# Optimization experiments

Measured on AMD Instinct MI355X. Metric: run time of the kernel, lower is better.

## Reference

```python
import jax, jax.numpy as jnp
import numpy as np

DIM = 320; HEADS = 8; DHEAD = 40; CTX_DIM = 768
INNER = HEADS * DHEAD; FF_INNER = 4 * DIM
B = 1; N = 4096; M = 77
SCALE = DHEAD ** -0.5


def setup_inputs() -> dict:
    key = jax.random.key(0)
    ks = jax.random.split(key, 16)
    p = lambda i, shape: jax.random.normal(ks[i], shape, dtype=jnp.float32) * 0.02
    return {
        "x": jax.random.normal(ks[0], (B, N, DIM), dtype=jnp.float32),
        "context": jax.random.normal(ks[1], (B, M, CTX_DIM), dtype=jnp.float32),
        "focused_attention_mask": jax.random.uniform(ks[2], (1, M, M), dtype=jnp.float32),
        "g1": jnp.ones((DIM,), jnp.float32), "b1": jnp.zeros((DIM,), jnp.float32),
        "g2": jnp.ones((DIM,), jnp.float32), "b2": jnp.zeros((DIM,), jnp.float32),
        "g3": jnp.ones((DIM,), jnp.float32), "b3": jnp.zeros((DIM,), jnp.float32),
        "Wq1": p(3, (DIM, INNER)), "Wk1": p(4, (DIM, INNER)), "Wv1": p(5, (DIM, INNER)),
        "Wo1": p(6, (INNER, DIM)), "bo1": jnp.zeros((DIM,), jnp.float32),
        "Wq2": p(7, (DIM, INNER)), "Wk2": p(8, (CTX_DIM, INNER)), "Wv2": p(9, (CTX_DIM, INNER)),
        "Wo2": p(10, (INNER, DIM)), "bo2": jnp.zeros((DIM,), jnp.float32),
        "Wff1": p(11, (DIM, 2 * FF_INNER)), "bff1": jnp.zeros((2 * FF_INNER,), jnp.float32),
        "Wff2": p(12, (FF_INNER, DIM)), "bff2": jnp.zeros((DIM,), jnp.float32),
        "use_fca": 1,
    }


def _ln(x, g, b):
    mu = x.mean(-1, keepdims=True)
    var = jnp.mean((x - mu) ** 2, -1, keepdims=True)
    return (x - mu) * jax.lax.rsqrt(var + 1e-5) * g + b


def _attn(xn, ctx, Wq, Wk, Wv, Wo, bo, fam, use_fca):
    b, n, _ = xn.shape
    heads = lambda t: t.reshape(b, t.shape[1], HEADS, DHEAD).transpose(0, 2, 1, 3)  # b h n d
    q, k, v = heads(xn @ Wq), heads(ctx @ Wk), heads(ctx @ Wv)
    sim = jnp.einsum('bhid,bhjd->bhij', q, k) * SCALE
    if use_fca:
        m = fam.shape[-1]  # fam: [1, m, m], batch must be 1 (repeat_interleave semantics)
        fw = jnp.einsum('bhqk,dk->bhqd', sim[..., :m], fam[0])
        fw = jnp.minimum(jnp.abs(fw), 1.0)
        fw = fw / (jnp.max(fw, axis=-1, keepdims=True) + 1e-6)
        fw = (fw > 0.6).astype(sim.dtype)
        sim = sim.at[..., :m].add((fw - 1.0) * 50.0)
    a = jax.nn.softmax(sim, axis=-1)
    o = jnp.einsum('bhij,bhjd->bhid', a, v).transpose(0, 2, 1, 3).reshape(b, n, INNER)
    return o @ Wo + bo


def reference(x, context, focused_attention_mask,
              g1, b1, g2, b2, g3, b3,
              Wq1, Wk1, Wv1, Wo1, bo1,
              Wq2, Wk2, Wv2, Wo2, bo2,
              Wff1, bff1, Wff2, bff2, use_fca):
    # attn1: self-attention (context=None in original -> use_fca forced to 0)
    h1 = _ln(x, g1, b1)
    x = _attn(h1, h1, Wq1, Wk1, Wv1, Wo1, bo1, None, 0) + x
    # attn2: cross-attention with focused-attention mask
    h2 = _ln(x, g2, b2)
    x = _attn(h2, context, Wq2, Wk2, Wv2, Wo2, bo2, focused_attention_mask, int(use_fca)) + x
    # GEGLU feed-forward
    h3 = _ln(x, g3, b3)
    proj = h3 @ Wff1 + bff1
    a_, gate = jnp.split(proj, 2, axis=-1)
    x = (a_ * jax.nn.gelu(gate, approximate=False)) @ Wff2 + bff2 + x
    return x
```

## Files before the change

### kernel.cpp

```cpp
#include <hip/hip_runtime.h>
#include <math.h>

typedef __bf16 bf16_t;
typedef __bf16 bf16x8 __attribute__((ext_vector_type(8)));
typedef __bf16 bf16x4 __attribute__((ext_vector_type(4)));
typedef float  f32x4  __attribute__((ext_vector_type(4)));
typedef _Float16 f16_t;
typedef _Float16 f16x4 __attribute__((ext_vector_type(4)));
typedef _Float16 f16x8 __attribute__((ext_vector_type(8)));
typedef __fp16 hf16x2 __attribute__((ext_vector_type(2)));

static constexpr float ATT_SCALE = 0.15811388300841897f;
static constexpr float SC2 = 0.22811031f;
static constexpr float LOG2E = 1.4426950408889634f;

__device__ __forceinline__ bf16_t f2b(float f) {
  unsigned u = __float_as_uint(f);
  u = (u + 0x7fffu + ((u >> 16) & 1u)) >> 16;
  unsigned short s = (unsigned short)u;
  bf16_t r;
  *(unsigned short*)&r = s;
  return r;
}
__device__ __forceinline__ float b2f(bf16_t b) {
  unsigned short s = *(const unsigned short*)&b;
  return __uint_as_float(((unsigned)s) << 16);
}
__device__ __forceinline__ void sto(float v, float* p)  { *p = v; }
__device__ __forceinline__ void sto(float v, bf16_t* p) { *p = f2b(v); }
__device__ __forceinline__ unsigned pkh2(float a, float b) {
  hf16x2 h = __builtin_amdgcn_cvt_pkrtz(a, b);
  return *(unsigned*)&h;
}

__global__ __launch_bounds__(256) void prep_kernel(
    const float* __restrict__ Wq1, const float* __restrict__ Wk1, const float* __restrict__ Wv1,
    const float* __restrict__ Wo1, const float* __restrict__ Wq2,
    const float* __restrict__ Wk2, const float* __restrict__ Wv2, const float* __restrict__ Wo2,
    const float* __restrict__ Wff1, const float* __restrict__ Wff2,
    const float* __restrict__ fam,
    bf16_t* __restrict__ wqkvt, bf16_t* __restrict__ wo1t, float* __restrict__ wkv2t,
    bf16_t* __restrict__ wo2t, bf16_t* __restrict__ wff1t, bf16_t* __restrict__ wff2t,
    bf16_t* __restrict__ wq2th, bf16_t* __restrict__ wq2tl,
    bf16_t* __restrict__ famh, bf16_t* __restrict__ faml,
    bf16_t* __restrict__ zpad)
{
  const int T1 = 960*320;
  const int T2 = T1 + 320*320;
  const int T3 = T2 + 768*640;
  const int T4 = T3 + 320*320;
  const int T5 = T4 + 2560*320;
  const int T6 = T5 + 320*1280;
  const int T7 = T6 + 320*320;
  const int T8 = T7 + 96*96;
  const int T9 = T8 + 135168;
  for (int i = blockIdx.x*256 + threadIdx.x; i < T9; i += gridDim.x*256) {
    if (i < T1) {
      int n = i / 320, k = i - n*320;
      float v = (n < 320) ? Wq1[k*320+n] * SC2
              : (n < 640) ? Wk1[k*320+n-320] : Wv1[k*320+n-640];
      wqkvt[i] = f2b(v);
    } else if (i < T2) {
      int e = i - T1; int n = e / 320, k = e - n*320;
      wo1t[e] = f2b(Wo1[k*320+n]);
    } else if (i < T3) {
      int e = i - T2; int n = e / 768, k = e - n*768;
      wkv2t[e] = (n < 320) ? Wk2[k*320+n] : Wv2[k*320+n-320];
    } else if (i < T4) {
      int e = i - T3; int n = e / 320, k = e - n*320;
      wo2t[e] = f2b(Wo2[k*320+n]);
    } else if (i < T5) {
      int e = i - T4; int n = e / 320, k = e - n*320;
      wff1t[e] = f2b(Wff1[(size_t)k*2560+n]);
    } else if (i < T6) {
      int e = i - T5; int n = e / 1280, k = e - n*1280;
      wff2t[e] = f2b(Wff2[k*320+n]);
    } else if (i < T7) {
      int e = i - T6; int n = e / 320, k = e - n*320;
      float v = Wq2[k*320+n];
      bf16_t h = f2b(v);
      wq2th[e] = h;
      wq2tl[e] = f2b(v - b2f(h));
    } else if (i < T8) {
      int e = i - T7; int d = e / 96, k = e - d*96;
      float v = (d < 77 && k < 77) ? fam[d*77 + k] : 0.f;
      bf16_t h = f2b(v);
      famh[e] = h;
      faml[e] = f2b(v - b2f(h));
    } else {
      zpad[i - T8] = f2b(0.f);
    }
  }
}

template<typename OT>
__global__ __launch_bounds__(256) void ln_kernel(
    const float* __restrict__ x, const float* __restrict__ g, const float* __restrict__ b,
    OT* __restrict__ out)
{
  const int lane = threadIdx.x & 63;
  const int row = blockIdx.x * 4 + (threadIdx.x >> 6);
  const float* xr = x + (size_t)row * 320;
  float v[5], s = 0.f, s2 = 0.f;
#pragma unroll
  for (int i = 0; i < 5; i++) { v[i] = xr[lane + i*64]; s += v[i]; s2 += v[i]*v[i]; }
#pragma unroll
  for (int o = 32; o; o >>= 1) { s += __shfl_xor(s, o); s2 += __shfl_xor(s2, o); }
  float mu = s * (1.f/320.f);
  float rs = rsqrtf(fmaxf(s2*(1.f/320.f) - mu*mu, 0.f) + 1e-5f);
#pragma unroll
  for (int i = 0; i < 5; i++) {
    int c = lane + i*64;
    sto((v[i]-mu)*rs*g[c] + b[c], &out[(size_t)row*320 + c]);
  }
}

__global__ __launch_bounds__(256) void ln2_split_kernel(
    const float* __restrict__ x, const float* __restrict__ g, const float* __restrict__ b,
    bf16_t* __restrict__ hi, bf16_t* __restrict__ lo)
{
  const int lane = threadIdx.x & 63;
  const int row = blockIdx.x * 4 + (threadIdx.x >> 6);
  const float* xr = x + (size_t)row * 320;
  float v[5], s = 0.f, s2 = 0.f;
#pragma unroll
  for (int i = 0; i < 5; i++) { v[i] = xr[lane + i*64]; s += v[i]; s2 += v[i]*v[i]; }
#pragma unroll
  for (int o = 32; o; o >>= 1) { s += __shfl_xor(s, o); s2 += __shfl_xor(s2, o); }
  float mu = s * (1.f/320.f);
  float rs = rsqrtf(fmaxf(s2*(1.f/320.f) - mu*mu, 0.f) + 1e-5f);
#pragma unroll
  for (int i = 0; i < 5; i++) {
    int c = lane + i*64;
    float y = (v[i]-mu)*rs*g[c] + b[c];
    bf16_t h = f2b(y);
    hi[(size_t)row*320 + c] = h;
    lo[(size_t)row*320 + c] = f2b(y - b2f(h));
  }
}

__global__ __launch_bounds__(256) void kv2_dot_kernel(
    const float* __restrict__ ctx, const float* __restrict__ wkv2t,
    bf16_t* __restrict__ k2h, bf16_t* __restrict__ k2l, bf16_t* __restrict__ v2t)
{
  const int gid = blockIdx.x*16 + (threadIdx.x >> 4);
  const int q = threadIdx.x & 15;
  const int m = gid / 640, n = gid - m*640;
  const float4* a = (const float4*)(ctx + (size_t)m*768);
  const float4* b = (const float4*)(wkv2t + (size_t)n*768);
  float acc = 0.f;
#pragma unroll
  for (int i = 0; i < 12; i++) {
    float4 av = a[i*16+q], bv = b[i*16+q];
    acc += av.x*bv.x + av.y*bv.y + av.z*bv.z + av.w*bv.w;
  }
#pragma unroll
  for (int o = 8; o; o >>= 1) acc += __shfl_xor(acc, o);
  if (q == 0) {
    if (n < 320) {
      int h = n / 40, d = n - h*40;
      int i = h*6144 + m*64 + d;
      bf16_t hh = f2b(acc);
      k2h[i] = hh;
      k2l[i] = f2b(acc - b2f(hh));
    } else {
      int n2 = n - 320; int h = n2 / 40, d = n2 - h*40;
      v2t[h*4608 + d*96 + m] = f2b(acc);
    }
  }
}

__global__ __launch_bounds__(256) void repack_vt_kernel(
    const bf16_t* __restrict__ qkvb, f16_t* __restrict__ vpack, bf16_t* __restrict__ kpack)
{
  __shared__ f16_t T[64*44];
  const int tid = threadIdx.x;
  const int t0 = blockIdx.x * 64, h = blockIdx.y;
  for (int e = tid; e < 320; e += 256) {
    int t = e / 5, c8 = (e - t*5) * 8;
    bf16x8 v = *(const bf16x8*)(qkvb + (size_t)(t0+t)*960 + 640 + h*40 + c8);
    f16_t* dst = &T[t*44 + c8];
#pragma unroll
    for (int j = 0; j < 8; j++) dst[j] = (f16_t)b2f(v[j]);
  }
  __syncthreads();
  for (int e = tid; e < 3072; e += 256) {
    int dt = e >> 10;
    int r  = e & 1023;
    int g2 = r >> 9, o = r & 511;
    int lane = o >> 3, j = o & 7;
    int qd = lane >> 4, ln = lane & 15;
    int d = dt*16 + ln;
    int key = g2*32 + ((j & 4) ? 16 : 0) + qd*4 + (j & 3);
    float val;
    if (d < 40)       val = (float)T[key*44 + d];
    else if (d == 40) val = 1.0f;
    else              val = 0.0f;
    vpack[(((size_t)h*3 + dt)*128 + (t0 >> 5) + g2)*512 + o] = (f16_t)val;
  }
  for (int e = tid; e < 2560; e += 256) {
    int g = e / 640, o = e - g*640;
    int key = t0 + g*16;
    bf16_t val;
    if (o < 512) {
      int lane = o >> 3, j = o & 7;
      int qd = lane >> 4, ln = lane & 15;
      val = qkvb[(size_t)(key + ln)*960 + 320 + h*40 + qd*8 + j];
    } else {
      int o2 = o - 512; int ln = o2 >> 3, j = o2 & 7;
      val = qkvb[(size_t)(key + ln)*960 + 320 + h*40 + 32 + j];
    }
    kpack[((size_t)h*256 + (t0 >> 4) + g)*640 + o] = val;
  }
}

__global__ __launch_bounds__(512, 4) void flash_self_kernel(
    const bf16_t* __restrict__ qkvb, const bf16_t* __restrict__ kpack,
    const f16_t* __restrict__ vpack,
    bf16_t* __restrict__ o1a)
{
  __shared__ float Red[12288];
  const int tid = threadIdx.x;
  const int w = tid >> 6, lane = tid & 63;
  const int ln = lane & 15, qd = lane >> 4;
  const int qh = w >> 2, kh = w & 3;
  const int h = blockIdx.x & 7;
  const int q0 = (blockIdx.x >> 3) * 64;

  const int kgbase = h*256 + kh*2;
  const int vgbase = h*384 + kh;
  const int lko = lane*8;

  bf16x8 zero8 = {};
  bf16x8 bq[2][2];
#pragma unroll
  for (int nt = 0; nt < 2; nt++) {
    const bf16_t* qp = qkvb + (size_t)(q0 + qh*32 + nt*16 + ln)*960 + h*40;
    bq[nt][0] = *(const bf16x8*)(qp + qd*8);
    bq[nt][1] = (qd == 0) ? *(const bf16x8*)(qp + 32) : zero8;
  }

  f32x4 zero4 = {0.f,0.f,0.f,0.f};
  f32x4 oacc[3][2];
#pragma unroll
  for (int a = 0; a < 3; a++)
#pragma unroll
    for (int b = 0; b < 2; b++) oacc[a][b] = zero4;

#define FS_LOADK(DST, K0)                                                       \
  {                                                                             \
    const bf16_t* kp_ = kpack + ((size_t)kgbase + ((K0) >> 4)) * 640;           \
    DST[0][0] = *(const bf16x8*)(kp_ + lko);                                    \
    DST[0][1] = (qd == 0) ? *(const bf16x8*)(kp_ + 512 + ln*8) : zero8;         \
    DST[1][0] = *(const bf16x8*)(kp_ + 640 + lko);                              \
    DST[1][1] = (qd == 0) ? *(const bf16x8*)(kp_ + 1152 + ln*8) : zero8;        \
  }

#define FS_LOADV(DST, K0)                                                       \
  {                                                                             \
    _Pragma("unroll")                                                           \
    for (int dt_ = 0; dt_ < 3; dt_++)                                           \
      DST[dt_] = *(const f16x8*)(vpack + ((size_t)vgbase + dt_*128 + ((K0) >> 5)) * 512 + lko); \
  }

#define FS_COMPUTE(KA, VA)                                                      \
  {                                                                             \
    _Pragma("unroll")                                                           \
    for (int nt = 0; nt < 2; nt++) {                                            \
      f32x4 s0 = __builtin_amdgcn_mfma_f32_16x16x32_bf16(KA[0][0], bq[nt][0], zero4, 0,0,0); \
      s0 = __builtin_amdgcn_mfma_f32_16x16x32_bf16(KA[0][1], bq[nt][1], s0, 0,0,0); \
      f32x4 s1 = __builtin_amdgcn_mfma_f32_16x16x32_bf16(KA[1][0], bq[nt][0], zero4, 0,0,0); \
      s1 = __builtin_amdgcn_mfma_f32_16x16x32_bf16(KA[1][1], bq[nt][1], s1, 0,0,0); \
      uint4 u_;                                                                 \
      u_.x = pkh2(__builtin_amdgcn_exp2f(s0[0]), __builtin_amdgcn_exp2f(s0[1])); \
      u_.y = pkh2(__builtin_amdgcn_exp2f(s0[2]), __builtin_amdgcn_exp2f(s0[3])); \
      u_.z = pkh2(__builtin_amdgcn_exp2f(s1[0]), __builtin_amdgcn_exp2f(s1[1])); \
      u_.w = pkh2(__builtin_amdgcn_exp2f(s1[2]), __builtin_amdgcn_exp2f(s1[3])); \
      f16x8 pb = *(f16x8*)&u_;                                                  \
      _Pragma("unroll")                                                         \
      for (int dt = 0; dt < 3; dt++)                                            \
        oacc[dt][nt] = __builtin_amdgcn_mfma_f32_16x16x32_f16(VA[dt], pb, oacc[dt][nt], 0,0,0); \
    }                                                                           \
  }

  bf16x8 ka[2][2], kb[2][2];
  f16x8 va[3], vb[3];
  FS_LOADK(ka, 0);
  FS_LOADV(va, 0);
#pragma unroll 1
  for (int it = 0; it < 32; it += 2) {
    const int k0 = it*128;
    FS_LOADK(kb, k0 + 128);
    FS_LOADV(vb, k0 + 128);
    FS_COMPUTE(ka, va);
    FS_LOADK(ka, (it + 2 < 32) ? (k0 + 256) : 0);
    FS_LOADV(va, (it + 2 < 32) ? (k0 + 256) : 0);
    FS_COMPUTE(kb, vb);
  }
#undef FS_LOADK
#undef FS_LOADV
#undef FS_COMPUTE

#pragma unroll
  for (int nt = 0; nt < 2; nt++)
#pragma unroll
    for (int dt = 0; dt < 3; dt++)
      *(f32x4*)&Red[((w*2 + nt)*3 + dt)*256 + ln*16 + qd*4] = oacc[dt][nt];
  __syncthreads();
  const int dgrp = tid & 7, lq = (tid >> 3) & 15, ntw = (tid >> 7) & 1, qh2 = tid >> 8;
  float l = Red[(((qh2*4 + 0)*2 + ntw)*3 + 2)*256 + lq*16 + 8]
          + Red[(((qh2*4 + 1)*2 + ntw)*3 + 2)*256 + lq*16 + 8]
          + Red[(((qh2*4 + 2)*2 + ntw)*3 + 2)*256 + lq*16 + 8]
          + Red[(((qh2*4 + 3)*2 + ntw)*3 + 2)*256 + lq*16 + 8];
  float inv = 1.f / l;
  bf16_t* obase = o1a + (size_t)(q0 + qh2*32 + ntw*16 + lq)*320 + h*40;
#pragma unroll
  for (int i = 0; i < 5; i++) {
    int d = dgrp + i*8;
    int dt = d >> 4, dr = d & 15;
    float o = Red[(((qh2*4 + 0)*2 + ntw)*3 + dt)*256 + lq*16 + dr]
            + Red[(((qh2*4 + 1)*2 + ntw)*3 + dt)*256 + lq*16 + dr]
            + Red[(((qh2*4 + 2)*2 + ntw)*3 + dt)*256 + lq*16 + dr]
            + Red[(((qh2*4 + 3)*2 + ntw)*3 + dt)*256 + lq*16 + dr];
    obase[d] = f2b(o * inv);
  }
}

__global__ __launch_bounds__(256) void attn_cross_kernel(
    const float* __restrict__ q2, const bf16_t* __restrict__ k2h, const bf16_t* __restrict__ k2l,
    const bf16_t* __restrict__ famh, const bf16_t* __restrict__ faml,
    const bf16_t* __restrict__ v2t, const int* __restrict__ use_fca,
    bf16_t* __restrict__ o2)
{
  __shared__ bf16_t SMh[4][16*96];
  __shared__ bf16_t SMl[4][16*96];
  __shared__ bf16_t PAs[4][16*96];
  const int tid = threadIdx.x;
  const int w = tid >> 6, lane = tid & 63;
  const int ln = lane & 15, qd = lane >> 4;
  const int h = blockIdx.x & 7;
  const int q0 = (blockIdx.x >> 3)*64 + w*16;
  const int fca = use_fca[0];
  bf16_t* smh = SMh[w];
  bf16_t* sml = SMl[w];
  bf16_t* pa  = PAs[w];

  {
    bf16x4 z = {};
    int q = lane >> 2, c = 80 + (lane & 3)*4;
    *(bf16x4*)&smh[q*96 + c] = z;
    *(bf16x4*)&sml[q*96 + c] = z;
    *(bf16x4*)&pa [q*96 + c] = z;
  }

  bf16x8 zero8 = {};
  bf16x8 aqh0, aql0, aqh1 = zero8, aql1 = zero8;
  {
    const float* qp = q2 + (size_t)(q0 + ln)*320 + h*40;
    float4 v0 = *(const float4*)(qp + qd*8);
    float4 v1 = *(const float4*)(qp + qd*8 + 4);
    float qv[8] = {v0.x,v0.y,v0.z,v0.w,v1.x,v1.y,v1.z,v1.w};
#pragma unroll
    for (int i = 0; i < 8; i++) {
      bf16_t hh = f2b(qv[i]);
      aqh0[i] = hh; aql0[i] = f2b(qv[i] - b2f(hh));
    }
    if (qd == 0) {
      float4 u0 = *(const float4*)(qp + 32);
      float4 u1 = *(const float4*)(qp + 36);
      float uv[8] = {u0.x,u0.y,u0.z,u0.w,u1.x,u1.y,u1.z,u1.w};
#pragma unroll
      for (int i = 0; i < 8; i++) {
        bf16_t hh = f2b(uv[i]);
        aqh1[i] = hh; aql1[i] = f2b(uv[i] - b2f(hh));
      }
    }
  }

  f32x4 zero4 = {0.f,0.f,0.f,0.f};
  float ss[5][4];
#pragma unroll
  for (int nt = 0; nt < 5; nt++) {
    const bf16_t* kb = k2h + ((size_t)h*96 + nt*16 + ln)*64 + qd*8;
    const bf16_t* kl = k2l + ((size_t)h*96 + nt*16 + ln)*64 + qd*8;
    bf16x8 kh0 = *(const bf16x8*)kb;
    bf16x8 kh1 = *(const bf16x8*)(kb + 32);
    bf16x8 kl0 = *(const bf16x8*)kl;
    bf16x8 kl1 = *(const bf16x8*)(kl + 32);
    f32x4 s;
    s = __builtin_amdgcn_mfma_f32_16x16x32_bf16(aqh0, kl0, zero4, 0, 0, 0);
    s = __builtin_amdgcn_mfma_f32_16x16x32_bf16(aql0, kh0, s, 0, 0, 0);
    s = __builtin_amdgcn_mfma_f32_16x16x32_bf16(aqh0, kh0, s, 0, 0, 0);
    s = __builtin_amdgcn_mfma_f32_16x16x32_bf16(aqh1, kl1, s, 0, 0, 0);
    s = __builtin_amdgcn_mfma_f32_16x16x32_bf16(aql1, kh1, s, 0, 0, 0);
    s = __builtin_amdgcn_mfma_f32_16x16x32_bf16(aqh1, kh1, s, 0, 0, 0);
#pragma unroll
    for (int r = 0; r < 4; r++) {
      float sv = s[r] * ATT_SCALE;
      ss[nt][r] = sv;
      bf16_t hh = f2b(sv);
      smh[(qd*4 + r)*96 + nt*16 + ln] = hh;
      sml[(qd*4 + r)*96 + nt*16 + ln] = f2b(sv - b2f(hh));
    }
  }

  f32x4 facc[5];
#pragma unroll
  for (int nt = 0; nt < 5; nt++) facc[nt] = zero4;
#pragma unroll
  for (int c = 0; c < 3; c++) {
    bf16x8 sah = *(const bf16x8*)&smh[ln*96 + c*32 + qd*8];
    bf16x8 sal = *(const bf16x8*)&sml[ln*96 + c*32 + qd*8];
#pragma unroll
    for (int nt = 0; nt < 5; nt++) {
      bf16x8 fh8 = *(const bf16x8*)(famh + ((size_t)(nt*16 + ln))*96 + c*32 + qd*8);
      bf16x8 fl8 = *(const bf16x8*)(faml + ((size_t)(nt*16 + ln))*96 + c*32 + qd*8);
      facc[nt] = __builtin_amdgcn_mfma_f32_16x16x32_bf16(sah, fl8, facc[nt], 0, 0, 0);
      facc[nt] = __builtin_amdgcn_mfma_f32_16x16x32_bf16(sal, fh8, facc[nt], 0, 0, 0);
      facc[nt] = __builtin_amdgcn_mfma_f32_16x16x32_bf16(sah, fh8, facc[nt], 0, 0, 0);
    }
  }

  float pr[5][4];
  if (fca) {
    float fwv[5][4], fm[4];
#pragma unroll
    for (int nt = 0; nt < 5; nt++)
#pragma unroll
      for (int r = 0; r < 4; r++) fwv[nt][r] = fminf(fabsf(facc[nt][r]), 1.f);
#pragma unroll
    for (int r = 0; r < 4; r++) {
      float m = fmaxf(fmaxf(fwv[0][r], fwv[1][r]), fmaxf(fwv[2][r], fmaxf(fwv[3][r], fwv[4][r])));
#pragma unroll
      for (int o = 8; o; o >>= 1) m = fmaxf(m, __shfl_xor(m, o));
      fm[r] = m;
    }
#pragma unroll
    for (int nt = 0; nt < 5; nt++)
#pragma unroll
      for (int r = 0; r < 4; r++) {
        float lg = ss[nt][r] - ((fwv[nt][r] > 0.6f*(fm[r] + 1e-6f)) ? 0.f : 50.f);
        pr[nt][r] = __builtin_amdgcn_exp2f(lg * LOG2E);
      }
  } else {
#pragma unroll
    for (int nt = 0; nt < 5; nt++)
#pragma unroll
      for (int r = 0; r < 4; r++)
        pr[nt][r] = __builtin_amdgcn_exp2f(ss[nt][r] * LOG2E);
  }
  if (ln >= 13) {
#pragma unroll
    for (int r = 0; r < 4; r++) pr[4][r] = 0.f;
  }
  float l_[4] = {0.f,0.f,0.f,0.f};
#pragma unroll
  for (int nt = 0; nt < 5; nt++)
#pragma unroll
    for (int r = 0; r < 4; r++) {
      l_[r] += pr[nt][r];
      pa[(qd*4 + r)*96 + nt*16 + ln] = f2b(pr[nt][r]);
    }
#pragma unroll
  for (int r = 0; r < 4; r++)
#pragma unroll
    for (int o = 8; o; o >>= 1) l_[r] += __shfl_xor(l_[r], o);

  f32x4 oacc[3];
#pragma unroll
  for (int nt = 0; nt < 3; nt++) oacc[nt] = zero4;
#pragma unroll
  for (int c = 0; c < 3; c++) {
    bf16x8 paf = *(const bf16x8*)&pa[ln*96 + c*32 + qd*8];
#pragma unroll
    for (int nt = 0; nt < 3; nt++) {
      bf16x8 vb = *(const bf16x8*)(v2t + ((size_t)h*48 + nt*16 + ln)*96 + c*32 + qd*8);
      oacc[nt] = __builtin_amdgcn_mfma_f32_16x16x32_bf16(paf, vb, oacc[nt], 0, 0, 0);
    }
  }
  float inv[4];
#pragma unroll
  for (int r = 0; r < 4; r++) inv[r] = 1.f / l_[r];
#pragma unroll
  for (int nt = 0; nt < 3; nt++) {
    int d = nt*16 + ln;
    if (d < 40) {
#pragma unroll
      for (int r = 0; r < 4; r++)
        o2[(size_t)(q0 + qd*4 + r)*320 + h*40 + d] = f2b(oacc[nt][r]*inv[r]);
    }
  }
}

template<int OUT_BF16>
__global__ __launch_bounds__(256) void gemm_bf16_kernel(
    const bf16_t* __restrict__ A, const bf16_t* __restrict__ Bt,
    const float* __restrict__ bias, const float* __restrict__ resid,
    void* __restrict__ Cout, int M, int N, int K)
{
  __shared__ bf16_t As[128][72];
  __shared__ bf16_t Bs[64][72];
  const int tid = threadIdx.x;
  const int m0 = blockIdx.x * 128, n0 = blockIdx.y * 64;
  const int w = tid >> 6, lane = tid & 63;
  const int wr = w >> 1, wc = w & 1;
  const int ln = lane & 15, qd = lane >> 4;
  f32x4 zero = {0.f, 0.f, 0.f, 0.f};
  f32x4 acc[4][2];
#pragma unroll
  for (int a = 0; a < 4; a++)
#pragma unroll
    for (int b = 0; b < 2; b++) acc[a][b] = zero;

  for (int k0 = 0; k0 < K; k0 += 64) {
    __syncthreads();
#pragma unroll
    for (int i = 0; i < 4; i++) {
      int vid = tid + i*256;
      int r = vid >> 3, c8 = (vid & 7) * 8;
      *(bf16x8*)&As[r][c8] = *(const bf16x8*)(A + (size_t)(m0+r)*K + k0 + c8);
    }
#pragma unroll
    for (int i = 0; i < 2; i++) {
      int vid = tid + i*256;
      int r = vid >> 3, c8 = (vid & 7) * 8;
      *(bf16x8*)&Bs[r][c8] = *(const bf16x8*)(Bt + (size_t)(n0+r)*K + k0 + c8);
    }
    __syncthreads();
#pragma unroll
    for (int c = 0; c < 2; c++) {
      bf16x8 af[4], bfr[2];
#pragma unroll
      for (int mt = 0; mt < 4; mt++)
        af[mt] = *(const bf16x8*)&As[wr*64 + mt*16 + ln][c*32 + qd*8];
#pragma unroll
      for (int nt = 0; nt < 2; nt++)
        bfr[nt] = *(const bf16x8*)&Bs[wc*32 + nt*16 + ln][c*32 + qd*8];
#pragma unroll
      for (int mt = 0; mt < 4; mt++)
#pragma unroll
        for (int nt = 0; nt < 2; nt++)
          acc[mt][nt] = __builtin_amdgcn_mfma_f32_16x16x32_bf16(af[mt], bfr[nt], acc[mt][nt], 0, 0, 0);
    }
  }
#pragma unroll
  for (int mt = 0; mt < 4; mt++)
#pragma unroll
    for (int nt = 0; nt < 2; nt++)
#pragma unroll
      for (int r = 0; r < 4; r++) {
        int gm = m0 + wr*64 + mt*16 + qd*4 + r;
        int gn = n0 + wc*32 + nt*16 + ln;
        float v = acc[mt][nt][r];
        if (bias)  v += bias[gn];
        if (resid) v += resid[(size_t)gm*N + gn];
        if (OUT_BF16) sto(v, &((bf16_t*)Cout)[(size_t)gm*N + gn]);
        else          sto(v, &((float*)Cout)[(size_t)gm*N + gn]);
      }
}

template<int OUT_BF16>
__global__ __launch_bounds__(256) void gemm_bf16_32_kernel(
    const bf16_t* __restrict__ A, const bf16_t* __restrict__ Bt,
    const float* __restrict__ bias, const float* __restrict__ resid,
    void* __restrict__ Cout, int M, int N, int K)
{
  __shared__ bf16_t As[32][72];
  __shared__ bf16_t Bs[64][72];
  const int tid = threadIdx.x;
  const int m0 = blockIdx.x * 32, n0 = blockIdx.y * 64;
  const int w = tid >> 6, lane = tid & 63;
  const int wr = w >> 1, wc = w & 1;
  const int ln = lane & 15, qd = lane >> 4;
  f32x4 zero = {0.f, 0.f, 0.f, 0.f};
  f32x4 acc[2];
  acc[0] = zero; acc[1] = zero;

  for (int k0 = 0; k0 < K; k0 += 64) {
    __syncthreads();
    {
      int r = tid >> 3, c8 = (tid & 7) * 8;
      *(bf16x8*)&As[r][c8] = *(const bf16x8*)(A + (size_t)(m0+r)*K + k0 + c8);
    }
#pragma unroll
    for (int i = 0; i < 2; i++) {
      int vid = tid + i*256;
      int r = vid >> 3, c8 = (vid & 7) * 8;
      *(bf16x8*)&Bs[r][c8] = *(const bf16x8*)(Bt + (size_t)(n0+r)*K + k0 + c8);
    }
    __syncthreads();
#pragma unroll
    for (int c = 0; c < 2; c++) {
      bf16x8 af = *(const bf16x8*)&As[wr*16 + ln][c*32 + qd*8];
#pragma unroll
      for (int nt = 0; nt < 2; nt++) {
        bf16x8 bfr = *(const bf16x8*)&Bs[wc*32 + nt*16 + ln][c*32 + qd*8];
        acc[nt] = __builtin_amdgcn_mfma_f32_16x16x32_bf16(af, bfr, acc[nt], 0, 0, 0);
      }
    }
  }
#pragma unroll
  for (int nt = 0; nt < 2; nt++)
#pragma unroll
    for (int r = 0; r < 4; r++) {
      int gm = m0 + wr*16 + qd*4 + r;
      int gn = n0 + wc*32 + nt*16 + ln;
      float v = acc[nt][r];
      if (bias)  v += bias[gn];
      if (resid) v += resid[(size_t)gm*N + gn];
      if (OUT_BF16) sto(v, &((bf16_t*)Cout)[(size_t)gm*N + gn]);
      else          sto(v, &((float*)Cout)[(size_t)gm*N + gn]);
    }
}

__global__ __launch_bounds__(256) void gemm3_32_kernel(
    const bf16_t* __restrict__ Ah, const bf16_t* __restrict__ Al,
    const bf16_t* __restrict__ Bth, const bf16_t* __restrict__ Btl,
    float* __restrict__ C, int M, int N, int K)
{
  __shared__ bf16_t Ash[32][72];
  __shared__ bf16_t Asl[32][72];
  __shared__ bf16_t Bsh[64][72];
  __shared__ bf16_t Bsl[64][72];
  const int tid = threadIdx.x;
  const int m0 = blockIdx.x * 32, n0 = blockIdx.y * 64;
  const int w = tid >> 6, lane = tid & 63;
  const int wr = w >> 1, wc = w & 1;
  const int ln = lane & 15, qd = lane >> 4;
  f32x4 zero = {0.f, 0.f, 0.f, 0.f};
  f32x4 acc[2];
  acc[0] = zero; acc[1] = zero;

  for (int k0 = 0; k0 < K; k0 += 64) {
    __syncthreads();
    {
      int r = tid >> 3, c8 = (tid & 7) * 8;
      *(bf16x8*)&Ash[r][c8] = *(const bf16x8*)(Ah + (size_t)(m0+r)*K + k0 + c8);
      *(bf16x8*)&Asl[r][c8] = *(const bf16x8*)(Al + (size_t)(m0+r)*K + k0 + c8);
    }
#pragma unroll
    for (int i = 0; i < 2; i++) {
      int vid = tid + i*256;
      int r = vid >> 3, c8 = (vid & 7) * 8;
      *(bf16x8*)&Bsh[r][c8] = *(const bf16x8*)(Bth + (size_t)(n0+r)*K + k0 + c8);
      *(bf16x8*)&Bsl[r][c8] = *(const bf16x8*)(Btl + (size_t)(n0+r)*K + k0 + c8);
    }
    __syncthreads();
#pragma unroll
    for (int c = 0; c < 2; c++) {
      bf16x8 afh = *(const bf16x8*)&Ash[wr*16 + ln][c*32 + qd*8];
      bf16x8 afl = *(const bf16x8*)&Asl[wr*16 + ln][c*32 + qd*8];
#pragma unroll
      for (int nt = 0; nt < 2; nt++) {
        bf16x8 bfh = *(const bf16x8*)&Bsh[wc*32 + nt*16 + ln][c*32 + qd*8];
        bf16x8 bfl = *(const bf16x8*)&Bsl[wc*32 + nt*16 + ln][c*32 + qd*8];
        acc[nt] = __builtin_amdgcn_mfma_f32_16x16x32_bf16(afh, bfl, acc[nt], 0, 0, 0);
        acc[nt] = __builtin_amdgcn_mfma_f32_16x16x32_bf16(afl, bfh, acc[nt], 0, 0, 0);
        acc[nt] = __builtin_amdgcn_mfma_f32_16x16x32_bf16(afh, bfh, acc[nt], 0, 0, 0);
      }
    }
  }
#pragma unroll
  for (int nt = 0; nt < 2; nt++)
#pragma unroll
    for (int r = 0; r < 4; r++) {
      int gm = m0 + wr*16 + qd*4 + r;
      int gn = n0 + wc*32 + nt*16 + ln;
      C[(size_t)gm*N + gn] = acc[nt][r];
    }
}

__global__ __launch_bounds__(256) void gemm_geglu_kernel(
    const bf16_t* __restrict__ A, const bf16_t* __restrict__ Bt,
    const float* __restrict__ bias, bf16_t* __restrict__ gg, int K)
{
  __shared__ bf16_t As[128][72];
  __shared__ bf16_t Ba[64][72];
  __shared__ bf16_t Bg[64][72];
  const int tid = threadIdx.x;
  const int m0 = blockIdx.x * 128, n0 = blockIdx.y * 64;
  const int w = tid >> 6, lane = tid & 63;
  const int wr = w >> 1, wc = w & 1;
  const int ln = lane & 15, qd = lane >> 4;
  f32x4 zero = {0.f, 0.f, 0.f, 0.f};
  f32x4 acca[4][2], accg[4][2];
#pragma unroll
  for (int a = 0; a < 4; a++)
#pragma unroll
    for (int b = 0; b < 2; b++) { acca[a][b] = zero; accg[a][b] = zero; }

  for (int k0 = 0; k0 < K; k0 += 64) {
    __syncthreads();
#pragma unroll
    for (int i = 0; i < 4; i++) {
      int vid = tid + i*256;
      int r = vid >> 3, c8 = (vid & 7) * 8;
      *(bf16x8*)&As[r][c8] = *(const bf16x8*)(A + (size_t)(m0+r)*K + k0 + c8);
    }
#pragma unroll
    for (int i = 0; i < 2; i++) {
      int vid = tid + i*256;
      int r = vid >> 3, c8 = (vid & 7) * 8;
      *(bf16x8*)&Ba[r][c8] = *(const bf16x8*)(Bt + (size_t)(n0+r)*K + k0 + c8);
      *(bf16x8*)&Bg[r][c8] = *(const bf16x8*)(Bt + (size_t)(n0+r+1280)*K + k0 + c8);
    }
    __syncthreads();
#pragma unroll
    for (int c = 0; c < 2; c++) {
      bf16x8 af[4], ba[2], bg[2];
#pragma unroll
      for (int mt = 0; mt < 4; mt++)
        af[mt] = *(const bf16x8*)&As[wr*64 + mt*16 + ln][c*32 + qd*8];
#pragma unroll
      for (int nt = 0; nt < 2; nt++) {
        ba[nt] = *(const bf16x8*)&Ba[wc*32 + nt*16 + ln][c*32 + qd*8];
        bg[nt] = *(const bf16x8*)&Bg[wc*32 + nt*16 + ln][c*32 + qd*8];
      }
#pragma unroll
      for (int mt = 0; mt < 4; mt++)
#pragma unroll
        for (int nt = 0; nt < 2; nt++) {
          acca[mt][nt] = __builtin_amdgcn_mfma_f32_16x16x32_bf16(af[mt], ba[nt], acca[mt][nt], 0, 0, 0);
          accg[mt][nt] = __builtin_amdgcn_mfma_f32_16x16x32_bf16(af[mt], bg[nt], accg[mt][nt], 0, 0, 0);
        }
    }
  }
#pragma unroll
  for (int mt = 0; mt < 4; mt++)
#pragma unroll
    for (int nt = 0; nt < 2; nt++)
#pragma unroll
      for (int r = 0; r < 4; r++) {
        int gm = m0 + wr*64 + mt*16 + qd*4 + r;
        int gn = n0 + wc*32 + nt*16 + ln;
        float va = acca[mt][nt][r] + bias[gn];
        float vg = accg[mt][nt][r] + bias[1280 + gn];
        float ge = 0.5f * vg * (1.f + erff(vg * 0.70710678118654752f));
        gg[(size_t)gm*1280 + gn] = f2b(va * ge);
      }
}

extern "C" void kernel_launch(void* const* d_in, const int* in_sizes, int n_in,
                              void* d_out, int out_size, void* d_ws, size_t ws_size,
                              hipStream_t stream)
{
  const float* x    = (const float*)d_in[0];
  const float* ctx  = (const float*)d_in[1];
  const float* fam  = (const float*)d_in[2];
  const float* g1   = (const float*)d_in[3];
  const float* b1   = (const float*)d_in[4];
  const float* g2   = (const float*)d_in[5];
  const float* b2   = (const float*)d_in[6];
  const float* g3   = (const float*)d_in[7];
  const float* b3   = (const float*)d_in[8];
  const float* Wq1  = (const float*)d_in[9];
  const float* Wk1  = (const float*)d_in[10];
  const float* Wv1  = (const float*)d_in[11];
  const float* Wo1  = (const float*)d_in[12];
  const float* bo1  = (const float*)d_in[13];
  const float* Wq2  = (const float*)d_in[14];
  const float* Wk2  = (const float*)d_in[15];
  const float* Wv2  = (const float*)d_in[16];
  const float* Wo2  = (const float*)d_in[17];
  const float* bo2  = (const float*)d_in[18];
  const float* Wff1 = (const float*)d_in[19];
  const float* bff1 = (const float*)d_in[20];
  const float* Wff2 = (const float*)d_in[21];
  const float* bff2 = (const float*)d_in[22];
  const int*   ufca = (const int*)d_in[23];

  char* ws = (char*)d_ws;
  bf16_t* qkvb = (bf16_t*)(ws + 0);
  f16_t*  vpack = (f16_t*)(ws + 7864320);
  bf16_t* kpack = (bf16_t*)(ws + 11010048);
  bf16_t* h1b  = (bf16_t*)(ws + 13631488);
  bf16_t* h2hi = (bf16_t*)(ws + 16252928);
  bf16_t* h2lo = (bf16_t*)(ws + 18874368);
  float*  x2   = (float*)(ws + 21495808);
  float*  q2   = (float*)(ws + 26738688);
  bf16_t* o1a  = (bf16_t*)(ws + 26738688);
  bf16_t* o2   = (bf16_t*)(ws + 32178688);
  float*  x3   = (float*)(ws + 34800128);
  bf16_t* h3b  = (bf16_t*)(ws + 40043008);
  bf16_t* wqkvt = (bf16_t*)(ws + 42664448);
  bf16_t* wo1t  = (bf16_t*)(ws + 43278848);
  float*  wkv2t = (float*)(ws + 43483648);
  bf16_t* wo2t  = (bf16_t*)(ws + 45449728);
  bf16_t* wff1t = (bf16_t*)(ws + 45654528);
  bf16_t* wff2t = (bf16_t*)(ws + 47292928);
  bf16_t* wq2th = (bf16_t*)(ws + 48374272);
  bf16_t* wq2tl = (bf16_t*)(ws + 48579072);
  bf16_t* famh  = (bf16_t*)(ws + 48783872);
  bf16_t* faml  = (bf16_t*)(ws + 48802304);
  bf16_t* k2h   = (bf16_t*)(ws + 48820736);
  bf16_t* k2l   = (bf16_t*)(ws + 48919040);
  bf16_t* v2t   = (bf16_t*)(ws + 49017344);
  bf16_t* gg   = (bf16_t*)(ws + 21495808);

  float* xout = (float*)d_out;

  prep_kernel<<<2048, 256, 0, stream>>>(Wq1, Wk1, Wv1, Wo1, Wq2, Wk2, Wv2, Wo2, Wff1, Wff2, fam,
                                        wqkvt, wo1t, wkv2t, wo2t, wff1t, wff2t, wq2th, wq2tl,
                                        famh, faml, k2h);
  ln_kernel<bf16_t><<<1024, 256, 0, stream>>>(x, g1, b1, h1b);
  gemm_bf16_kernel<1><<<dim3(32,15), 256, 0, stream>>>(h1b, wqkvt, nullptr, nullptr, qkvb, 4096, 960, 320);
  repack_vt_kernel<<<dim3(64,8), 256, 0, stream>>>(qkvb, vpack, kpack);
  flash_self_kernel<<<512, 512, 0, stream>>>(qkvb, kpack, vpack, o1a);
  gemm_bf16_32_kernel<0><<<dim3(128,5), 256, 0, stream>>>(o1a, wo1t, bo1, x, x2, 4096, 320, 320);
  ln2_split_kernel<<<1024, 256, 0, stream>>>(x2, g2, b2, h2hi, h2lo);
  gemm3_32_kernel<<<dim3(128,5), 256, 0, stream>>>(h2hi, h2lo, wq2th, wq2tl, q2, 4096, 320, 320);
  kv2_dot_kernel<<<3080, 256, 0, stream>>>(ctx, wkv2t, k2h, k2l, v2t);
  attn_cross_kernel<<<512, 256, 0, stream>>>(q2, k2h, k2l, famh, faml, v2t, ufca, o2);
  gemm_bf16_32_kernel<0><<<dim3(128,5), 256, 0, stream>>>(o2, wo2t, bo2, x2, x3, 4096, 320, 320);
  ln_kernel<bf16_t><<<1024, 256, 0, stream>>>(x3, g3, b3, h3b);
  gemm_geglu_kernel<<<dim3(32,20), 256, 0, stream>>>(h3b, wff1t, bff1, gg, 320);
  gemm_bf16_32_kernel<0><<<dim3(128,5), 256, 0, stream>>>(gg, wff2t, bff2, x3, xout, 4096, 320, 1280);
}
```

Baseline: 264.7 us.

## Use LDS-tiled transposes in weight prep and cache weight rows in kv2 dot

The weight-prep kernel now transposes each weight matrix in 64x64 tiles staged through shared memory, so both the global reads and the global writes are coalesced instead of using strided per-element gathers. The fam padding and zero fill move to a separate set of blocks. The kv2 dot kernel now loads a 16-row slab of the KV weight into shared memory once per block and reuses it across up to 20 context rows, cutting redundant global weight reads and launching 160 blocks instead of 3080. The cost is more shared memory per block and fewer blocks for the small context projection.

```diff
diff --git a/kernel.cpp b/kernel.cpp
--- a/kernel.cpp
+++ b/kernel.cpp
@@ -33,7 +33,7 @@
   return *(unsigned*)&h;
 }
 
-__global__ __launch_bounds__(256) void prep_kernel(
+__global__ __launch_bounds__(256) void prep_t_kernel(
     const float* __restrict__ Wq1, const float* __restrict__ Wk1, const float* __restrict__ Wv1,
     const float* __restrict__ Wo1, const float* __restrict__ Wq2,
     const float* __restrict__ Wk2, const float* __restrict__ Wv2, const float* __restrict__ Wo2,
@@ -45,50 +45,79 @@
     bf16_t* __restrict__ famh, bf16_t* __restrict__ faml,
     bf16_t* __restrict__ zpad)
 {
-  const int T1 = 960*320;
-  const int T2 = T1 + 320*320;
-  const int T3 = T2 + 768*640;
-  const int T4 = T3 + 320*320;
-  const int T5 = T4 + 2560*320;
-  const int T6 = T5 + 320*1280;
-  const int T7 = T6 + 320*320;
-  const int T8 = T7 + 96*96;
-  const int T9 = T8 + 135168;
-  for (int i = blockIdx.x*256 + threadIdx.x; i < T9; i += gridDim.x*256) {
-    if (i < T1) {
-      int n = i / 320, k = i - n*320;
-      float v = (n < 320) ? Wq1[k*320+n] * SC2
-              : (n < 640) ? Wk1[k*320+n-320] : Wv1[k*320+n-640];
-      wqkvt[i] = f2b(v);
-    } else if (i < T2) {
-      int e = i - T1; int n = e / 320, k = e - n*320;
-      wo1t[e] = f2b(Wo1[k*320+n]);
-    } else if (i < T3) {
-      int e = i - T2; int n = e / 768, k = e - n*768;
-      wkv2t[e] = (n < 320) ? Wk2[k*320+n] : Wv2[k*320+n-320];
-    } else if (i < T4) {
-      int e = i - T3; int n = e / 320, k = e - n*320;
-      wo2t[e] = f2b(Wo2[k*320+n]);
-    } else if (i < T5) {
-      int e = i - T4; int n = e / 320, k = e - n*320;
-      wff1t[e] = f2b(Wff1[(size_t)k*2560+n]);
-    } else if (i < T6) {
-      int e = i - T5; int n = e / 1280, k = e - n*1280;
-      wff2t[e] = f2b(Wff2[k*320+n]);
-    } else if (i < T7) {
-      int e = i - T6; int n = e / 320, k = e - n*320;
-      float v = Wq2[k*320+n];
+  const int b = blockIdx.x;
+  const int tid = threadIdx.x;
+
+  if (b >= 570) {
+    for (int idx = (b - 570)*256 + tid; idx < 9216 + 135168; idx += 64*256) {
+      if (idx < 9216) {
+        int d = idx / 96, k = idx - d*96;
+        float v = (d < 77 && k < 77) ? fam[d*77 + k] : 0.f;
+        bf16_t h = f2b(v);
+        famh[idx] = h;
+        faml[idx] = f2b(v - b2f(h));
+      } else {
+        zpad[idx - 9216] = f2b(0.f);
+      }
+    }
+    return;
+  }
+
+  __shared__ float T[64][65];
+  const float* src; int S, O, n0, k0, mode;
+  float scale = 1.f;
+  bf16_t* outb = nullptr; float* outf = nullptr;
+  int nadj;
+
+  if (b < 75) {
+    int tn = b / 5, tk = b - tn*5;
+    n0 = tn*64; k0 = tk*64; S = 320; O = 320; mode = 0; outb = wqkvt;
+    if (n0 < 320)      { src = Wq1; nadj = n0;       scale = SC2; }
+    else if (n0 < 640) { src = Wk1; nadj = n0 - 320; }
+    else               { src = Wv1; nadj = n0 - 640; }
+  } else if (b < 100) {
+    int b2 = b - 75; int tn = b2 / 5, tk = b2 - tn*5;
+    n0 = tn*64; k0 = tk*64; S = 320; O = 320; mode = 0; outb = wo1t; src = Wo1; nadj = n0;
+  } else if (b < 220) {
+    int b2 = b - 100; int tn = b2 / 12, tk = b2 - tn*12;
+    n0 = tn*64; k0 = tk*64; S = 320; O = 768; mode = 1; outf = wkv2t;
+    if (n0 < 320) { src = Wk2; nadj = n0; } else { src = Wv2; nadj = n0 - 320; }
+  } else if (b < 245) {
+    int b2 = b - 220; int tn = b2 / 5, tk = b2 - tn*5;
+    n0 = tn*64; k0 = tk*64; S = 320; O = 320; mode = 0; outb = wo2t; src = Wo2; nadj = n0;
+  } else if (b < 445) {
+    int b2 = b - 245; int tn = b2 / 5, tk = b2 - tn*5;
+    n0 = tn*64; k0 = tk*64; S = 2560; O = 320; mode = 0; outb = wff1t; src = Wff1; nadj = n0;
+  } else if (b < 545) {
+    int b2 = b - 445; int tn = b2 / 20, tk = b2 - tn*20;
+    n0 = tn*64; k0 = tk*64; S = 320; O = 1280; mode = 0; outb = wff2t; src = Wff2; nadj = n0;
+  } else {
+    int b2 = b - 545; int tn = b2 / 5, tk = b2 - tn*5;
+    n0 = tn*64; k0 = tk*64; S = 320; O = 320; mode = 2; src = Wq2; nadj = n0;
+  }
+
+  const int r4 = tid >> 6;
+  const int c  = tid & 63;
+  const float* srcp = src + nadj;
+#pragma unroll
+  for (int i = 0; i < 16; i++) {
+    int r = i*4 + r4;
+    T[c][r] = srcp[(size_t)(k0 + r)*S + c] * scale;
+  }
+  __syncthreads();
+#pragma unroll
+  for (int i = 0; i < 16; i++) {
+    int r = i*4 + r4;
+    float v = T[r][c];
+    size_t oi = (size_t)(n0 + r)*O + k0 + c;
+    if (mode == 0) {
+      outb[oi] = f2b(v);
+    } else if (mode == 1) {
+      outf[oi] = v;
+    } else {
       bf16_t h = f2b(v);
-      wq2th[e] = h;
-      wq2tl[e] = f2b(v - b2f(h));
-    } else if (i < T8) {
-      int e = i - T7; int d = e / 96, k = e - d*96;
-      float v = (d < 77 && k < 77) ? fam[d*77 + k] : 0.f;
-      bf16_t h = f2b(v);
-      famh[e] = h;
-      faml[e] = f2b(v - b2f(h));
-    } else {
-      zpad[i - T8] = f2b(0.f);
+      wq2th[oi] = h;
+      wq2tl[oi] = f2b(v - b2f(h));
     }
   }
 }
@@ -143,29 +172,40 @@
     const float* __restrict__ ctx, const float* __restrict__ wkv2t,
     bf16_t* __restrict__ k2h, bf16_t* __restrict__ k2l, bf16_t* __restrict__ v2t)
 {
-  const int gid = blockIdx.x*16 + (threadIdx.x >> 4);
-  const int q = threadIdx.x & 15;
-  const int m = gid / 640, n = gid - m*640;
-  const float4* a = (const float4*)(ctx + (size_t)m*768);
-  const float4* b = (const float4*)(wkv2t + (size_t)n*768);
-  float acc = 0.f;
-#pragma unroll
-  for (int i = 0; i < 12; i++) {
-    float4 av = a[i*16+q], bv = b[i*16+q];
-    acc += av.x*bv.x + av.y*bv.y + av.z*bv.z + av.w*bv.w;
-  }
-#pragma unroll
-  for (int o = 8; o; o >>= 1) acc += __shfl_xor(acc, o);
-  if (q == 0) {
-    if (n < 320) {
-      int h = n / 40, d = n - h*40;
-      int i = h*6144 + m*64 + d;
-      bf16_t hh = f2b(acc);
-      k2h[i] = hh;
-      k2l[i] = f2b(acc - b2f(hh));
-    } else {
-      int n2 = n - 320; int h = n2 / 40, d = n2 - h*40;
-      v2t[h*4608 + d*96 + m] = f2b(acc);
+  __shared__ float4 Bs[16][193];
+  const int tid = threadIdx.x;
+  const int nb = blockIdx.x % 40, ms = blockIdx.x / 40;
+  const int n0 = nb*16;
+  for (int e = tid; e < 16*192; e += 256) {
+    int row = e / 192, c4 = e - row*192;
+    Bs[row][c4] = *(const float4*)(wkv2t + (size_t)(n0+row)*768 + c4*4);
+  }
+  __syncthreads();
+  const int g = tid >> 4, q = tid & 15;
+  const int mlo = ms*20;
+  const int mhi = (mlo + 20 > 77) ? 77 : mlo + 20;
+  for (int m = mlo; m < mhi; m++) {
+    const float4* a = (const float4*)(ctx + (size_t)m*768);
+    float acc = 0.f;
+#pragma unroll
+    for (int i = 0; i < 12; i++) {
+      float4 av = a[i*16+q], bv = Bs[g][i*16+q];
+      acc += av.x*bv.x + av.y*bv.y + av.z*bv.z + av.w*bv.w;
+    }
+#pragma unroll
+    for (int o = 8; o; o >>= 1) acc += __shfl_xor(acc, o);
+    if (q == 0) {
+      int n = n0 + g;
+      if (n < 320) {
+        int h = n / 40, d = n - h*40;
+        int idx = h*6144 + m*64 + d;
+        bf16_t hh = f2b(acc);
+        k2h[idx] = hh;
+        k2l[idx] = f2b(acc - b2f(hh));
+      } else {
+        int n2 = n - 320; int h = n2 / 40, d = n2 - h*40;
+        v2t[h*4608 + d*96 + m] = f2b(acc);
+      }
     }
   }
 }
@@ -799,9 +839,9 @@
 
   float* xout = (float*)d_out;
 
-  prep_kernel<<<2048, 256, 0, stream>>>(Wq1, Wk1, Wv1, Wo1, Wq2, Wk2, Wv2, Wo2, Wff1, Wff2, fam,
-                                        wqkvt, wo1t, wkv2t, wo2t, wff1t, wff2t, wq2th, wq2tl,
-                                        famh, faml, k2h);
+  prep_t_kernel<<<634, 256, 0, stream>>>(Wq1, Wk1, Wv1, Wo1, Wq2, Wk2, Wv2, Wo2, Wff1, Wff2, fam,
+                                         wqkvt, wo1t, wkv2t, wo2t, wff1t, wff2t, wq2th, wq2tl,
+                                         famh, faml, k2h);
   ln_kernel<bf16_t><<<1024, 256, 0, stream>>>(x, g1, b1, h1b);
   gemm_bf16_kernel<1><<<dim3(32,15), 256, 0, stream>>>(h1b, wqkvt, nullptr, nullptr, qkvb, 4096, 960, 320);
   repack_vt_kernel<<<dim3(64,8), 256, 0, stream>>>(qkvb, vpack, kpack);
@@ -809,7 +849,7 @@
   gemm_bf16_32_kernel<0><<<dim3(128,5), 256, 0, stream>>>(o1a, wo1t, bo1, x, x2, 4096, 320, 320);
   ln2_split_kernel<<<1024, 256, 0, stream>>>(x2, g2, b2, h2hi, h2lo);
   gemm3_32_kernel<<<dim3(128,5), 256, 0, stream>>>(h2hi, h2lo, wq2th, wq2tl, q2, 4096, 320, 320);
-  kv2_dot_kernel<<<3080, 256, 0, stream>>>(ctx, wkv2t, k2h, k2l, v2t);
+  kv2_dot_kernel<<<160, 256, 0, stream>>>(ctx, wkv2t, k2h, k2l, v2t);
   attn_cross_kernel<<<512, 256, 0, stream>>>(q2, k2h, k2l, famh, faml, v2t, ufca, o2);
   gemm_bf16_32_kernel<0><<<dim3(128,5), 256, 0, stream>>>(o2, wo2t, bo2, x2, x3, 4096, 320, 320);
   ln_kernel<bf16_t><<<1024, 256, 0, stream>>>(x3, g3, b3, h3b);
```

New measurement: 261.6 us. Within noise of the previous version (-1.2%).
